# Performance work log

Hardware: AMD Instinct MI355X
Metric: run time of the kernel (lower is better)

The kernel has to match this reference:

```python
import jax, jax.numpy as jnp
import numpy as np

K = 16  # topK from config


def setup_inputs() -> dict:
    key = jax.random.key(0)
    k1, k2 = jax.random.split(key)
    predictions = jax.random.uniform(k1, (8, 256, 8), dtype=jnp.float32)
    ref_imgs = jax.random.uniform(k2, (8, 3, 192, 192), dtype=jnp.float32)
    return {"predictions": predictions, "ref_imgs": ref_imgs}


def _dist_loss(predictions, ref_imgs):
    bs, L, _ = predictions.shape
    ch, H, W = ref_imgs.shape[1], ref_imgs.shape[2], ref_imgs.shape[3]
    img_size = W  # original uses ref_imgs.shape[-1] for both axes
    pos = predictions[:, :, :2]  # (bs, L, 2), normalized (x, y) in [0, 1]

    # --- nearest grid_sample (align_corners=False, padding zeros) ---
    # Faithful to the original einops mixup: flat sample i uses image i % bs
    # and grid point preds.reshape(bs*L, 2)[i].
    grid = pos.reshape(bs * L, 2)
    img_idx = jnp.arange(bs * L) % bs
    # unnormalize: pix = ((2g - 1) + 1) * S / 2 - 0.5 = g * S - 0.5
    ix = jnp.round(grid[:, 0] * W - 0.5).astype(jnp.int32)
    iy = jnp.round(grid[:, 1] * H - 0.5).astype(jnp.int32)
    inb = ((ix >= 0) & (ix < W) & (iy >= 0) & (iy < H)).astype(ref_imgs.dtype)
    ixc = jnp.clip(ix, 0, W - 1)
    iyc = jnp.clip(iy, 0, H - 1)
    pooled_flat = ref_imgs[img_idx, :, iyc, ixc] * inb[:, None]  # (bs*L, ch)
    # pooled_colors rearranged '(L bs) ch 1 1 -> bs L ch' with flat order (L outer, bs inner)
    pooled = pooled_flat.reshape(L, bs, ch).transpose(1, 0, 2)  # (bs, L, ch)

    # --- per-pixel squared color distance, sum over channels ---
    # ||ref - pooled||^2 = ||ref||^2 - 2<ref, pooled> + ||pooled||^2 (avoids (bs,L,ch,H,W))
    ref_sq = jnp.sum(ref_imgs * ref_imgs, axis=1)  # (bs, H, W)
    cross = jnp.einsum('bchw,blc->blhw', ref_imgs, pooled)  # (bs, L, H, W)
    pooled_sq = jnp.sum(pooled * pooled, axis=-1)  # (bs, L)
    similar = ref_sq[:, None] - 2.0 * cross + pooled_sq[:, :, None, None]

    # --- K most-similar pixel locations ---
    _, idx = jax.lax.top_k(-similar.reshape(bs, L, H * W), K)  # smallest K
    tgt_x = (idx % img_size).astype(pos.dtype) / img_size
    tgt_y = (idx // img_size).astype(pos.dtype) / img_size
    tgt = jnp.stack([tgt_x, tgt_y], axis=-1)  # (bs, L, K, 2)
    tgt_down = jnp.roll(tgt, shift=1, axis=1)

    # --- closest candidate of the previous stroke (positions detached) ---
    pd = jax.lax.stop_gradient(pos)[:, :, None, :]  # (bs, L, 1, 2)
    dist_down = jnp.sum((pd - tgt_down) ** 2, axis=-1)  # (bs, L, K)
    closest = jnp.argmin(dist_down, axis=-1)  # (bs, L)
    final_tgt = jnp.take_along_axis(tgt_down, closest[:, :, None, None], axis=2)[:, :, 0, :]

    loss = jnp.sum((pos[:, 1:] - final_tgt[:, 1:]) ** 2, axis=-1)  # (bs, L-1)
    return jnp.mean(loss)


def reference(predictions, ref_imgs):
    return _dist_loss(predictions, ref_imgs)
```

## Files before the change

kernel.cpp:

```cpp
#include <hip/hip_runtime.h>
#include <stdint.h>

#define BS 8
#define HH 192
#define WW 192
#define HW (HH*WW)
#define KK 16
#define SITES 9216
#define NQ 4
#define NW 16
#define SEGSZ 32
#define UCAP 256
#define PAD_FILT 4e-5f

typedef unsigned long long u64;


__device__ __forceinline__ uint32_t fkey(float f) {
    uint32_t u = __float_as_uint(f);
    uint32_t mask = (uint32_t)((int32_t)u >> 31) | 0x80000000u;
    return u ^ mask;
}
__device__ __forceinline__ float inv_fkey(uint32_t v) {
    uint32_t u = (v & 0x80000000u) ? (v ^ 0x80000000u) : ~v;
    return __uint_as_float(u);
}

__device__ __forceinline__ u64 umin64(u64 a, u64 b) { return a < b ? a : b; }

__device__ __forceinline__ uint32_t mbcnt64(u64 m) {
    return __builtin_amdgcn_mbcnt_hi((uint32_t)(m >> 32),
            __builtin_amdgcn_mbcnt_lo((uint32_t)m, 0));
}

__device__ __forceinline__ u64 wave_min_u64(u64 v) {
    #pragma unroll
    for (int off = 32; off >= 1; off >>= 1) {
        uint32_t lo = (uint32_t)v, hi = (uint32_t)(v >> 32);
        lo = __shfl_xor(lo, off, 64);
        hi = __shfl_xor(hi, off, 64);
        u64 o = ((u64)hi << 32) | lo;
        v = umin64(v, o);
    }
    return v;
}

__device__ __forceinline__ void insert64(u64 (&kept)[KK], u64 key) {
    #pragma unroll
    for (int j = KK - 1; j >= 1; --j) {
        u64 a = kept[j - 1];
        u64 mn = umin64(kept[j], key);
        kept[j] = (key < a) ? a : mn;
    }
    kept[0] = umin64(kept[0], key);
}

__device__ __forceinline__ float exact_rsq(float a, float b, float c) {
    return __fadd_rn(__fadd_rn(__fmul_rn(a, a), __fmul_rn(b, b)), __fmul_rn(c, c));
}
__device__ __forceinline__ float exact_sim(float c0, float c1, float c2, float rsq, float4 pq) {
    float cr = __fadd_rn(__fadd_rn(__fmul_rn(c0, pq.x), __fmul_rn(c1, pq.y)), __fmul_rn(c2, pq.z));
    return __fadd_rn(__fsub_rn(rsq, __fmul_rn(2.0f, cr)), pq.w);
}

#define LOSS_STEP(gmv)                                                   \
{                                                                        \
    uint32_t idxv = (uint32_t)(gmv);                                     \
    float tx = (float)(idxv % WW) / 192.0f;                              \
    float ty = (float)(idxv / WW) / 192.0f;                              \
    float ddx = __fsub_rn(px1, tx);                                      \
    float ddy = __fsub_rn(py1, ty);                                      \
    float dd = __fadd_rn(__fmul_rn(ddx, ddx), __fmul_rn(ddy, ddy));      \
    if (dd < dmin) { dmin = dd; btx = tx; bty = ty; }                    \
}

__global__ __launch_bounds__(1024, 8) void fused_kernel(const float* __restrict__ pred,
                                                        const float* __restrict__ ref,
                                                        float* __restrict__ partial) {
    __shared__ uint32_t mxseg[4096];
    __shared__ uint32_t compactb[NQ * UCAP];
    __shared__ uint32_t scnts[NQ * NW];
    __shared__ float4 spool[NQ];
    __shared__ float shq[NQ];

    int tid  = threadIdx.x;
    int lane = tid & 63;
    int wid  = tid >> 6;
    int b  = blockIdx.x & 7;
    int qg = blockIdx.x >> 3;

    if (tid < NQ) {
        int l = qg * NQ + tid;
        int i = l * BS + b;
        int b2 = i >> 8, l2 = i & 255;
        const float* pr = pred + ((b2 * 256 + l2) * 8);
        float x = pr[0], y = pr[1];
        float fx = rintf(__fsub_rn(__fmul_rn(x, 192.0f), 0.5f));
        float fy = rintf(__fsub_rn(__fmul_rn(y, 192.0f), 0.5f));
        int ix = (int)fx, iy = (int)fy;
        int inb = (ix >= 0 && ix < WW && iy >= 0 && iy < HH) ? 1 : 0;
        int ixc = min(max(ix, 0), WW - 1);
        int iyc = min(max(iy, 0), HH - 1);
        float m = (float)inb;
        const float* img = ref + b * 3 * HW + iyc * WW + ixc;
        float p0 = __fmul_rn(img[0], m);
        float p1 = __fmul_rn(img[HW], m);
        float p2 = __fmul_rn(img[2 * HW], m);
        float psq = __fadd_rn(__fadd_rn(__fmul_rn(p0, p0), __fmul_rn(p1, p1)),
                              __fmul_rn(p2, p2));
        spool[tid] = make_float4(p0, p1, p2, psq);
    }
    __syncthreads();

    const float4* p0g = (const float4*)(ref + (size_t)b * 3 * HW);
    float qx[NQ], qy[NQ], qz[NQ];
    #pragma unroll
    for (int q = 0; q < NQ; ++q) {
        float4 s = spool[q];
        qx[q] = s.x; qy[q] = s.y; qz[q] = s.z;
    }

    float md0 = -3.4e38f, md1 = -3.4e38f, md2 = -3.4e38f, md3 = -3.4e38f;
    #pragma unroll 1
    for (int it = 0; it < 4; ++it) {
        int site = tid + it * 1024;
        float4 a0 = p0g[site], a1 = p0g[site + SITES], a2 = p0g[site + 2 * SITES];
        #define SAMP(comp)                                                              \
        {                                                                               \
            float nr = -0.5f * fmaf(a2.comp, a2.comp, fmaf(a1.comp, a1.comp,            \
                              a0.comp * a0.comp));                                      \
            float d0_ = fmaf(a2.comp, qz[0], fmaf(a1.comp, qy[0], fmaf(a0.comp, qx[0], nr))); \
            float d1_ = fmaf(a2.comp, qz[1], fmaf(a1.comp, qy[1], fmaf(a0.comp, qx[1], nr))); \
            float d2_ = fmaf(a2.comp, qz[2], fmaf(a1.comp, qy[2], fmaf(a0.comp, qx[2], nr))); \
            float d3_ = fmaf(a2.comp, qz[3], fmaf(a1.comp, qy[3], fmaf(a0.comp, qx[3], nr))); \
            md0 = fmaxf(md0, d0_); md1 = fmaxf(md1, d1_);                               \
            md2 = fmaxf(md2, d2_); md3 = fmaxf(md3, d3_);                               \
        }
        SAMP(x) SAMP(y) SAMP(z) SAMP(w)
        #undef SAMP
    }
    mxseg[0 * 1024 + tid] = fkey(-md0);
    mxseg[1 * 1024 + tid] = fkey(-md1);
    mxseg[2 * 1024 + tid] = fkey(-md2);
    mxseg[3 * 1024 + tid] = fkey(-md3);
    __syncthreads();

    if (wid < NQ) {
        uint32_t v[16];
        #pragma unroll
        for (int j = 0; j < 16; ++j) v[j] = mxseg[wid * 1024 + lane + 64 * j];
        uint32_t lo = 0u, hi = 0xFFFFFFFFu;
        #pragma unroll 1
        for (int t = 0; t < 32; ++t) {
            uint32_t mid = lo + ((hi - lo) >> 1);
            int c = 0;
            #pragma unroll
            for (int j = 0; j < 16; ++j) c += (int)__popcll(__ballot(v[j] <= mid));
            if (c >= KK) hi = mid; else lo = mid + 1;
        }
        float hval = -inv_fkey(hi) - PAD_FILT;
        if (qg == 63 && wid == 3) hval = 3.0e38f;
        if (lane == 0) shq[wid] = hval;
    }
    __syncthreads();

    float hq0 = shq[0], hq1 = shq[1], hq2 = shq[2], hq3 = shq[3];
    uint32_t scq0 = 0, scq1 = 0, scq2 = 0, scq3 = 0;

    #pragma unroll 1
    for (int it = 0; it < 9; ++it) {
        int site = tid + it * 1024;
        float4 a0 = p0g[site], a1 = p0g[site + SITES], a2 = p0g[site + 2 * SITES];
        int base = site * 4;

        float nrx = -0.5f * fmaf(a2.x, a2.x, fmaf(a1.x, a1.x, a0.x * a0.x));
        float nry = -0.5f * fmaf(a2.y, a2.y, fmaf(a1.y, a1.y, a0.y * a0.y));
        float nrz = -0.5f * fmaf(a2.z, a2.z, fmaf(a1.z, a1.z, a0.z * a0.z));
        float nrw = -0.5f * fmaf(a2.w, a2.w, fmaf(a1.w, a1.w, a0.w * a0.w));

        #define QPUSH(qi, hqv, scq)                                                     \
        {                                                                               \
            float d0 = fmaf(a2.x, qz[qi], fmaf(a1.x, qy[qi], fmaf(a0.x, qx[qi], nrx))); \
            float d1 = fmaf(a2.y, qz[qi], fmaf(a1.y, qy[qi], fmaf(a0.y, qx[qi], nry))); \
            float d2 = fmaf(a2.z, qz[qi], fmaf(a1.z, qy[qi], fmaf(a0.z, qx[qi], nrz))); \
            float d3 = fmaf(a2.w, qz[qi], fmaf(a1.w, qy[qi], fmaf(a0.w, qx[qi], nrw))); \
            u64 m0 = __ballot(d0 >= hqv);                                               \
            u64 m1 = __ballot(d1 >= hqv);                                               \
            u64 m2 = __ballot(d2 >= hqv);                                               \
            u64 m3 = __ballot(d3 >= hqv);                                               \
            if (m0 | m1 | m2 | m3) {                    \
                uint32_t sb = ((qi) * NW + wid) * SEGSZ;                                \
                uint32_t c = scq;                                                       \
                if (d0 >= hqv) { uint32_t s = c + mbcnt64(m0);                          \
                                 if (s < SEGSZ) mxseg[sb + s] = (uint32_t)(base + 0); } \
                c += (uint32_t)__popcll(m0);                                            \
                if (d1 >= hqv) { uint32_t s = c + mbcnt64(m1);                          \
                                 if (s < SEGSZ) mxseg[sb + s] = (uint32_t)(base + 1); } \
                c += (uint32_t)__popcll(m1);                                            \
                if (d2 >= hqv) { uint32_t s = c + mbcnt64(m2);                          \
                                 if (s < SEGSZ) mxseg[sb + s] = (uint32_t)(base + 2); } \
                c += (uint32_t)__popcll(m2);                                            \
                if (d3 >= hqv) { uint32_t s = c + mbcnt64(m3);                          \
                                 if (s < SEGSZ) mxseg[sb + s] = (uint32_t)(base + 3); } \
                c += (uint32_t)__popcll(m3);                                            \
                scq = c;                                                                \
            }                                                                           \
        }
        QPUSH(0, hq0, scq0) QPUSH(1, hq1, scq1) QPUSH(2, hq2, scq2) QPUSH(3, hq3, scq3)
        #undef QPUSH
    }
    if (lane == 0) {
        scnts[0 * NW + wid] = scq0; scnts[1 * NW + wid] = scq1;
        scnts[2 * NW + wid] = scq2; scnts[3 * NW + wid] = scq3;
    }
    __syncthreads();

    if (wid < NQ) {
        int l  = qg * NQ + wid;
        int bl = b * 256 + l;
        if (l == 255) {
            if (lane == 0) partial[bl] = 0.0f;
        } else {
            bool ovf = false;
            uint32_t pref = 0;
            #pragma unroll
            for (int j = 0; j < NW; ++j) {
                uint32_t c = scnts[wid * NW + j];
                ovf = ovf || (c > SEGSZ);
                uint32_t cc = min(c, (uint32_t)SEGSZ);
                if (lane < cc && pref + lane < UCAP)
                    compactb[wid * UCAP + pref + lane] =
                        mxseg[(wid * NW + j) * SEGSZ + lane];
                pref += cc;
            }
            uint32_t U = pref;
            if (U > UCAP) ovf = true;

            float px1 = pred[(size_t)(bl + 1) * 8 + 0];
            float py1 = pred[(size_t)(bl + 1) * 8 + 1];
            float4 pqv = spool[wid];
            const float* rb = ref + (size_t)b * 3 * HW;

            if (!ovf) {
                uint32_t kh0, kh1, kh2, kh3, kl0, kl1, kl2, kl3;
                #define LOADJ(jj, kh, kl)                                               \
                {                                                                       \
                    uint32_t e = (jj) * 64 + lane;                                      \
                    uint32_t h_ = 0xFFFFFFFFu, l_ = 0xFFFFFFFFu;                        \
                    if (e < U) {                                                        \
                        uint32_t pidx = compactb[wid * UCAP + e];                       \
                        float c0v = rb[pidx], c1v = rb[pidx + HW], c2v = rb[pidx + 2 * HW]; \
                        float rs = exact_rsq(c0v, c1v, c2v);                            \
                        float sx = exact_sim(c0v, c1v, c2v, rs, pqv);                   \
                        h_ = fkey(sx); l_ = pidx;                                       \
                    }                                                                   \
                    kh = h_; kl = l_;                                                   \
                }
                LOADJ(0, kh0, kl0) LOADJ(1, kh1, kl1) LOADJ(2, kh2, kl2) LOADJ(3, kh3, kl3)
                #undef LOADJ

                uint32_t lo = 0u, hi = 0xFFFFFFFFu;
                #pragma unroll 1
                for (int t = 0; t < 32; ++t) {
                    uint32_t mid = lo + ((hi - lo) >> 1);
                    int c = (int)__popcll(__ballot(kh0 <= mid))
                          + (int)__popcll(__ballot(kh1 <= mid))
                          + (int)__popcll(__ballot(kh2 <= mid))
                          + (int)__popcll(__ballot(kh3 <= mid));
                    if (c >= KK) hi = mid; else lo = mid + 1;
                }
                uint32_t Hh = hi;
                int c1 = (int)__popcll(__ballot(kh0 < Hh))
                       + (int)__popcll(__ballot(kh1 < Hh))
                       + (int)__popcll(__ballot(kh2 < Hh))
                       + (int)__popcll(__ballot(kh3 < Hh));
                int need = KK - c1;
                u64 e0 = __ballot(kh0 == Hh), e1 = __ballot(kh1 == Hh);
                u64 e2 = __ballot(kh2 == Hh), e3 = __ballot(kh3 == Hh);
                lo = 0u; hi = 0xFFFFFFFFu;
                #pragma unroll 1
                for (int t = 0; t < 32; ++t) {
                    uint32_t mid = lo + ((hi - lo) >> 1);
                    int c = (int)__popcll(e0 & __ballot(kl0 <= mid))
                          + (int)__popcll(e1 & __ballot(kl1 <= mid))
                          + (int)__popcll(e2 & __ballot(kl2 <= mid))
                          + (int)__popcll(e3 & __ballot(kl3 <= mid));
                    if (c >= need) hi = mid; else lo = mid + 1;
                }
                uint32_t Lh = hi;

                uint32_t bd = 0xFFFFFFFFu, bh = 0xFFFFFFFFu, bo = 0xFFFFFFFFu;
                #define SELJ(kh, kl)                                                    \
                {                                                                       \
                    bool sel = (kh < Hh) || (kh == Hh && kl <= Lh);                     \
                    if (sel) {                                                          \
                        uint32_t idxv = kl;                                             \
                        float tx = (float)(idxv % WW) / 192.0f;                         \
                        float ty = (float)(idxv / WW) / 192.0f;                         \
                        float ddx = __fsub_rn(px1, tx);                                 \
                        float ddy = __fsub_rn(py1, ty);                                 \
                        float dd = __fadd_rn(__fmul_rn(ddx, ddx), __fmul_rn(ddy, ddy)); \
                        uint32_t db = __float_as_uint(dd);         \
                        bool lt = (db < bd) ||                                          \
                                  (db == bd && (kh < bh || (kh == bh && kl < bo)));     \
                        if (lt) { bd = db; bh = kh; bo = kl; }                          \
                    }                                                                   \
                }
                SELJ(kh0, kl0) SELJ(kh1, kl1) SELJ(kh2, kl2) SELJ(kh3, kl3)
                #undef SELJ
                #pragma unroll
                for (int off = 32; off >= 1; off >>= 1) {
                    uint32_t od = __shfl_xor(bd, off, 64);
                    uint32_t oh = __shfl_xor(bh, off, 64);
                    uint32_t oo = __shfl_xor(bo, off, 64);
                    bool lt = (od < bd) ||
                              (od == bd && (oh < bh || (oh == bh && oo < bo)));
                    if (lt) { bd = od; bh = oh; bo = oo; }
                }
                if (lane == 0) {
                    uint32_t idxv = bo;
                    float tx = (float)(idxv % WW) / 192.0f;
                    float ty = (float)(idxv / WW) / 192.0f;
                    float ex = __fsub_rn(px1, tx);
                    float ey = __fsub_rn(py1, ty);
                    partial[bl] = __fadd_rn(__fmul_rn(ex, ex), __fmul_rn(ey, ey));
                }
            } else {
                float dmin = 3.4e38f, btx = 0.0f, bty = 0.0f;
                u64 kept16[KK];
                #pragma unroll
                for (int j = 0; j < KK; ++j) kept16[j] = ~0ull;
                const float4* pg = (const float4*)rb;
                #pragma unroll 1
                for (int st = lane; st < SITES; st += 64) {
                    float4 a0 = pg[st], a1 = pg[st + SITES], a2 = pg[st + 2 * SITES];
                    int base = st * 4;
                    #define FB(comp, ei)                                                \
                    {                                                                   \
                        float rs = exact_rsq(a0.comp, a1.comp, a2.comp);                \
                        float sx = exact_sim(a0.comp, a1.comp, a2.comp, rs, pqv);       \
                        u64 key = ((u64)fkey(sx) << 32) | (uint32_t)(base + (ei));      \
                        if (key < kept16[KK - 1]) insert64(kept16, key);                \
                    }
                    FB(x, 0) FB(y, 1) FB(z, 2) FB(w, 3)
                    #undef FB
                }
                #pragma unroll 1
                for (int rnd = 0; rnd < 16; ++rnd) {
                    u64 gm = wave_min_u64(kept16[0]);
                    if (kept16[0] == gm) {
                        #pragma unroll
                        for (int j = 0; j < KK - 1; ++j) kept16[j] = kept16[j + 1];
                        kept16[KK - 1] = ~0ull;
                    }
                    LOSS_STEP(gm)
                }
                if (lane == 0) {
                    float ex = __fsub_rn(px1, btx);
                    float ey = __fsub_rn(py1, bty);
                    partial[bl] = __fadd_rn(__fmul_rn(ex, ex), __fmul_rn(ey, ey));
                }
            }
        }
    }
}

__global__ __launch_bounds__(256) void reduce_kernel(const float* __restrict__ partial,
                                                     float* __restrict__ out) {
    __shared__ double sred[256];
    double a = 0.0;
    #pragma unroll
    for (int i = 0; i < 8; ++i) a += (double)partial[i * 256 + threadIdx.x];
    sred[threadIdx.x] = a;
    __syncthreads();
    for (int s = 128; s > 0; s >>= 1) {
        if (threadIdx.x < s) sred[threadIdx.x] += sred[threadIdx.x + s];
        __syncthreads();
    }
    if (threadIdx.x == 0) out[0] = (float)(sred[0] / 2040.0);
}

extern "C" void kernel_launch(void* const* d_in, const int* in_sizes, int n_in,
                              void* d_out, int out_size, void* d_ws, size_t ws_size,
                              hipStream_t stream) {
    const float* pred = (const float*)d_in[0];
    const float* ref  = (const float*)d_in[1];
    float* out = (float*)d_out;

    float* partial = (float*)d_ws;

    fused_kernel <<<512, 1024, 0, stream>>>(pred, ref, partial);
    reduce_kernel<<<  1,  256, 0, stream>>>(partial, out);
}
```

Measured before the change: 90.51 us.

## Prefetch candidate-pass loads, compute exact keys at push time, trim binary searches

```diff
diff --git a/kernel.cpp b/kernel.cpp
--- a/kernel.cpp
+++ b/kernel.cpp
@@ -77,11 +77,12 @@
 __global__ __launch_bounds__(1024, 8) void fused_kernel(const float* __restrict__ pred,
                                                         const float* __restrict__ ref,
                                                         float* __restrict__ partial) {
-    __shared__ uint32_t mxseg[4096];
-    __shared__ uint32_t compactb[NQ * UCAP];
+    __shared__ u64 seg64[NQ * NW * SEGSZ];
+    __shared__ u64 comp64[NQ * UCAP];
     __shared__ uint32_t scnts[NQ * NW];
     __shared__ float4 spool[NQ];
     __shared__ float shq[NQ];
+    uint32_t* mx = (uint32_t*)seg64;
 
     int tid  = threadIdx.x;
     int lane = tid & 63;
@@ -139,19 +140,24 @@
         SAMP(x) SAMP(y) SAMP(z) SAMP(w)
         #undef SAMP
     }
-    mxseg[0 * 1024 + tid] = fkey(-md0);
-    mxseg[1 * 1024 + tid] = fkey(-md1);
-    mxseg[2 * 1024 + tid] = fkey(-md2);
-    mxseg[3 * 1024 + tid] = fkey(-md3);
+    mx[0 * 1024 + tid] = fkey(-md0);
+    mx[1 * 1024 + tid] = fkey(-md1);
+    mx[2 * 1024 + tid] = fkey(-md2);
+    mx[3 * 1024 + tid] = fkey(-md3);
+
+    float4 n0, n1, n2;
+    if (wid >= NQ) {
+        n0 = p0g[tid]; n1 = p0g[tid + SITES]; n2 = p0g[tid + 2 * SITES];
+    }
     __syncthreads();
 
     if (wid < NQ) {
         uint32_t v[16];
         #pragma unroll
-        for (int j = 0; j < 16; ++j) v[j] = mxseg[wid * 1024 + lane + 64 * j];
+        for (int j = 0; j < 16; ++j) v[j] = mx[wid * 1024 + lane + 64 * j];
         uint32_t lo = 0u, hi = 0xFFFFFFFFu;
         #pragma unroll 1
-        for (int t = 0; t < 32; ++t) {
+        for (int t = 0; t < 20; ++t) {
             uint32_t mid = lo + ((hi - lo) >> 1);
             int c = 0;
             #pragma unroll
@@ -161,53 +167,63 @@
         float hval = -inv_fkey(hi) - PAD_FILT;
         if (qg == 63 && wid == 3) hval = 3.0e38f;
         if (lane == 0) shq[wid] = hval;
+        n0 = p0g[tid]; n1 = p0g[tid + SITES]; n2 = p0g[tid + 2 * SITES];
     }
     __syncthreads();
 
     float hq0 = shq[0], hq1 = shq[1], hq2 = shq[2], hq3 = shq[3];
     uint32_t scq0 = 0, scq1 = 0, scq2 = 0, scq3 = 0;
+    int site3 = tid;
 
     #pragma unroll 1
     for (int it = 0; it < 9; ++it) {
-        int site = tid + it * 1024;
-        float4 a0 = p0g[site], a1 = p0g[site + SITES], a2 = p0g[site + 2 * SITES];
-        int base = site * 4;
+        float4 a0 = n0, a1 = n1, a2 = n2;
+        int sn = (it < 8) ? (site3 + 1024) : site3;
+        n0 = p0g[sn]; n1 = p0g[sn + SITES]; n2 = p0g[sn + 2 * SITES];
+        int base = site3 * 4;
 
         float nrx = -0.5f * fmaf(a2.x, a2.x, fmaf(a1.x, a1.x, a0.x * a0.x));
         float nry = -0.5f * fmaf(a2.y, a2.y, fmaf(a1.y, a1.y, a0.y * a0.y));
         float nrz = -0.5f * fmaf(a2.z, a2.z, fmaf(a1.z, a1.z, a0.z * a0.z));
         float nrw = -0.5f * fmaf(a2.w, a2.w, fmaf(a1.w, a1.w, a0.w * a0.w));
 
+        #define PUSHC(cv0, cv1, cv2, dj, mj, eidx)                                      \
+            if (dj >= hqv_) {                                                           \
+                uint32_t s_ = c + mbcnt64(mj);                                          \
+                if (s_ < SEGSZ) {                                                       \
+                    float rs_ = exact_rsq(cv0, cv1, cv2);                               \
+                    float sx_ = exact_sim(cv0, cv1, cv2, rs_, pqv_);                    \
+                    seg64[sb + s_] = ((u64)fkey(sx_) << 32) | (uint32_t)(base + eidx);  \
+                }                                                                       \
+            }                                                                           \
+            c += (uint32_t)__popcll(mj);
+
         #define QPUSH(qi, hqv, scq)                                                     \
         {                                                                               \
+            float hqv_ = hqv;                                                           \
             float d0 = fmaf(a2.x, qz[qi], fmaf(a1.x, qy[qi], fmaf(a0.x, qx[qi], nrx))); \
             float d1 = fmaf(a2.y, qz[qi], fmaf(a1.y, qy[qi], fmaf(a0.y, qx[qi], nry))); \
             float d2 = fmaf(a2.z, qz[qi], fmaf(a1.z, qy[qi], fmaf(a0.z, qx[qi], nrz))); \
             float d3 = fmaf(a2.w, qz[qi], fmaf(a1.w, qy[qi], fmaf(a0.w, qx[qi], nrw))); \
-            u64 m0 = __ballot(d0 >= hqv);                                               \
-            u64 m1 = __ballot(d1 >= hqv);                                               \
-            u64 m2 = __ballot(d2 >= hqv);                                               \
-            u64 m3 = __ballot(d3 >= hqv);                                               \
+            u64 m0 = __ballot(d0 >= hqv_);                                              \
+            u64 m1 = __ballot(d1 >= hqv_);                                              \
+            u64 m2 = __ballot(d2 >= hqv_);                                              \
+            u64 m3 = __ballot(d3 >= hqv_);                                              \
             if (m0 | m1 | m2 | m3) {                    \
+                float4 pqv_ = spool[qi];                                                \
                 uint32_t sb = ((qi) * NW + wid) * SEGSZ;                                \
                 uint32_t c = scq;                                                       \
-                if (d0 >= hqv) { uint32_t s = c + mbcnt64(m0);                          \
-                                 if (s < SEGSZ) mxseg[sb + s] = (uint32_t)(base + 0); } \
-                c += (uint32_t)__popcll(m0);                                            \
-                if (d1 >= hqv) { uint32_t s = c + mbcnt64(m1);                          \
-                                 if (s < SEGSZ) mxseg[sb + s] = (uint32_t)(base + 1); } \
-                c += (uint32_t)__popcll(m1);                                            \
-                if (d2 >= hqv) { uint32_t s = c + mbcnt64(m2);                          \
-                                 if (s < SEGSZ) mxseg[sb + s] = (uint32_t)(base + 2); } \
-                c += (uint32_t)__popcll(m2);                                            \
-                if (d3 >= hqv) { uint32_t s = c + mbcnt64(m3);                          \
-                                 if (s < SEGSZ) mxseg[sb + s] = (uint32_t)(base + 3); } \
-                c += (uint32_t)__popcll(m3);                                            \
+                PUSHC(a0.x, a1.x, a2.x, d0, m0, 0)                                      \
+                PUSHC(a0.y, a1.y, a2.y, d1, m1, 1)                                      \
+                PUSHC(a0.z, a1.z, a2.z, d2, m2, 2)                                      \
+                PUSHC(a0.w, a1.w, a2.w, d3, m3, 3)                                      \
                 scq = c;                                                                \
             }                                                                           \
         }
         QPUSH(0, hq0, scq0) QPUSH(1, hq1, scq1) QPUSH(2, hq2, scq2) QPUSH(3, hq3, scq3)
         #undef QPUSH
+        #undef PUSHC
+        site3 = sn;
     }
     if (lane == 0) {
         scnts[0 * NW + wid] = scq0; scnts[1 * NW + wid] = scq1;
@@ -229,8 +245,8 @@
                 ovf = ovf || (c > SEGSZ);
                 uint32_t cc = min(c, (uint32_t)SEGSZ);
                 if (lane < cc && pref + lane < UCAP)
-                    compactb[wid * UCAP + pref + lane] =
-                        mxseg[(wid * NW + j) * SEGSZ + lane];
+                    comp64[wid * UCAP + pref + lane] =
+                        seg64[(wid * NW + j) * SEGSZ + lane];
                 pref += cc;
             }
             uint32_t U = pref;
@@ -243,18 +259,15 @@
 
             if (!ovf) {
                 uint32_t kh0, kh1, kh2, kh3, kl0, kl1, kl2, kl3;
-                #define LOADJ(jj, kh, kl)                                               \
-                {                                                                       \
-                    uint32_t e = (jj) * 64 + lane;                                      \
-                    uint32_t h_ = 0xFFFFFFFFu, l_ = 0xFFFFFFFFu;                        \
-                    if (e < U) {                                                        \
-                        uint32_t pidx = compactb[wid * UCAP + e];                       \
-                        float c0v = rb[pidx], c1v = rb[pidx + HW], c2v = rb[pidx + 2 * HW]; \
-                        float rs = exact_rsq(c0v, c1v, c2v);                            \
-                        float sx = exact_sim(c0v, c1v, c2v, rs, pqv);                   \
-                        h_ = fkey(sx); l_ = pidx;                                       \
-                    }                                                                   \
-                    kh = h_; kl = l_;                                                   \
+                #define LOADJ(jj, kh, kl)                                      \
+                {                                                              \
+                    uint32_t e = (jj) * 64 + lane;                             \
+                    uint32_t h_ = 0xFFFFFFFFu, l_ = 0xFFFFFFFFu;               \
+                    if (e < U) {                                               \
+                        u64 v_ = comp64[wid * UCAP + e];                       \
+                        h_ = (uint32_t)(v_ >> 32); l_ = (uint32_t)v_;          \
+                    }                                                          \
+                    kh = h_; kl = l_;                                          \
                 }
                 LOADJ(0, kh0, kl0) LOADJ(1, kh1, kl1) LOADJ(2, kh2, kl2) LOADJ(3, kh3, kl3)
                 #undef LOADJ
@@ -274,20 +287,25 @@
                        + (int)__popcll(__ballot(kh1 < Hh))
                        + (int)__popcll(__ballot(kh2 < Hh))
                        + (int)__popcll(__ballot(kh3 < Hh));
-                int need = KK - c1;
                 u64 e0 = __ballot(kh0 == Hh), e1 = __ballot(kh1 == Hh);
                 u64 e2 = __ballot(kh2 == Hh), e3 = __ballot(kh3 == Hh);
-                lo = 0u; hi = 0xFFFFFFFFu;
-                #pragma unroll 1
-                for (int t = 0; t < 32; ++t) {
-                    uint32_t mid = lo + ((hi - lo) >> 1);
-                    int c = (int)__popcll(e0 & __ballot(kl0 <= mid))
-                          + (int)__popcll(e1 & __ballot(kl1 <= mid))
-                          + (int)__popcll(e2 & __ballot(kl2 <= mid))
-                          + (int)__popcll(e3 & __ballot(kl3 <= mid));
-                    if (c >= need) hi = mid; else lo = mid + 1;
-                }
-                uint32_t Lh = hi;
+                int ec = (int)__popcll(e0) + (int)__popcll(e1)
+                       + (int)__popcll(e2) + (int)__popcll(e3);
+                int need = KK - c1;
+                uint32_t Lh = 0xFFFFFFFFu;
+                if (ec != need) {
+                    lo = 0u; hi = 0xFFFFFFFFu;
+                    #pragma unroll 1
+                    for (int t = 0; t < 32; ++t) {
+                        uint32_t mid = lo + ((hi - lo) >> 1);
+                        int c = (int)__popcll(e0 & __ballot(kl0 <= mid))
+                              + (int)__popcll(e1 & __ballot(kl1 <= mid))
+                              + (int)__popcll(e2 & __ballot(kl2 <= mid))
+                              + (int)__popcll(e3 & __ballot(kl3 <= mid));
+                        if (c >= need) hi = mid; else lo = mid + 1;
+                    }
+                    Lh = hi;
+                }
 
                 uint32_t bd = 0xFFFFFFFFu, bh = 0xFFFFFFFFu, bo = 0xFFFFFFFFu;
                 #define SELJ(kh, kl)                                                    \
```

Measured after the change: 143.9 us. 1.59x slower.
